# Kernel tuning notes

Measured on AMD Instinct MI355X. Metric: run time of the kernel, lower is better.

The kernel has to match this reference:

```python
import jax, jax.numpy as jnp
import numpy as np

N, E, D_IN, H, NSEG, SEG = 40000, 640000, 127, 128, 512, 64
D0 = D_IN + 1  # node features + batch-indicator column


def setup_inputs() -> dict:
    ks = jax.random.split(jax.random.key(0), 12)
    def w(k, i, o):
        return jax.random.normal(k, (i, o), jnp.float32) / np.float32(np.sqrt(i))
    return dict(
        x=jax.random.normal(ks[0], (N, D_IN), jnp.float32),
        ei=jax.random.randint(ks[1], (2, E), 0, N, jnp.int32),
        ew=jax.random.uniform(ks[2], (E,), jnp.float32),
        batches=jax.random.randint(ks[3], (NSEG * SEG,), 0, N, jnp.int32),
        lens=jnp.arange(NSEG + 1, dtype=jnp.int32) * SEG,  # CSR offsets, 512 segments of 64
        gin_w0=w(ks[4], D0, H), gin_b0=jnp.zeros((H,), jnp.float32),
        gin_w1=w(ks[5], H, H), gin_b1=jnp.zeros((H,), jnp.float32),
        gin_w2=w(ks[6], H, H), gin_b2=jnp.zeros((H,), jnp.float32),
        r_w1=w(ks[7], 3 * H, H), r_b1=jnp.zeros((H,), jnp.float32),
        ln1_g=jnp.ones((H,), jnp.float32), ln1_b=jnp.zeros((H,), jnp.float32),
        r_w2=w(ks[8], H, H), r_b2=jnp.zeros((H,), jnp.float32),
        ln2_g=jnp.ones((H,), jnp.float32), ln2_b=jnp.zeros((H,), jnp.float32),
        r_w3=w(ks[9], H, 1), r_b3=jnp.zeros((1,), jnp.float32),
    )


def _layernorm(v, g, b, eps=1e-5):
    m = jnp.mean(v, -1, keepdims=True)
    var = jnp.mean((v - m) ** 2, -1, keepdims=True)
    return (v - m) * jax.lax.rsqrt(var + eps) * g + b


def _gin_layer(h, src, dst, ew, w, b):
    # GINConv with eps=0: MLP((1+eps)*h + sum_{j->i} ew_ji * h_j), MLP = Linear+ReLU
    agg = jax.ops.segment_sum(ew[:, None] * h[src], dst, num_segments=N)
    return jax.nn.relu((h + agg) @ w + b)


def reference(x, ei, ew, batches, lens,
              gin_w0, gin_b0, gin_w1, gin_b1, gin_w2, gin_b2,
              r_w1, r_b1, ln1_g, ln1_b, r_w2, r_b2, ln2_g, ln2_b, r_w3, r_b3):
    src, dst = ei[0], ei[1]
    # batch indicator feature
    bf = jnp.zeros((N, 1), x.dtype).at[batches].set(1.0)
    h = jnp.concatenate([x, bf], axis=1)  # [N, D0]
    for w_, b_ in ((gin_w0, gin_b0), (gin_w1, gin_b1), (gin_w2, gin_b2)):
        h = _gin_layer(h, src, dst, ew, w_, b_)
    # MultiPool: gather per-subgraph nodes then mean/min/max segment reductions
    seg = jnp.searchsorted(lens, jnp.arange(NSEG * SEG, dtype=jnp.int32), side='right') - 1
    src_e = h[batches]  # [total, H]
    counts = (lens[1:] - lens[:-1]).astype(h.dtype)[:, None]
    mean_p = jax.ops.segment_sum(src_e, seg, num_segments=NSEG) / counts
    min_p = jax.ops.segment_min(src_e, seg, num_segments=NSEG)
    max_p = jax.ops.segment_max(src_e, seg, num_segments=NSEG)
    z = jnp.concatenate([mean_p, min_p, max_p], axis=1)  # [NSEG, 3H]
    # readout: Linear, ReLU, LN, Linear, LN, ReLU, Linear
    z = _layernorm(jax.nn.relu(z @ r_w1 + r_b1), ln1_g, ln1_b)
    z = jax.nn.relu(_layernorm(z @ r_w2 + r_b2, ln2_g, ln2_b))
    return z @ r_w3 + r_b3  # logits [NSEG, 1]
```

## Files before the change

kernel.cpp:

```cpp
#include <hip/hip_runtime.h>
#include <hip/hip_fp16.h>

#define NN   40000
#define EE   640000
#define DIN  127
#define HH   128
#define NSEGS 512
#define SEGSZ 64
#define CAP  64
#define NB_ELL 625
#define NB_H0  10000

typedef unsigned int uint;
typedef unsigned short ushort;
typedef _Float16 f16;
typedef __attribute__((ext_vector_type(8))) _Float16 f16x8;
typedef __attribute__((ext_vector_type(4))) float f32x4;

__device__ __forceinline__ float h2f_lo(uint v) {
    __half_raw r; r.x = (ushort)(v & 0xffff); return __half2float(__half(r));
}
__device__ __forceinline__ float h2f_hi(uint v) {
    __half_raw r; r.x = (ushort)(v >> 16); return __half2float(__half(r));
}
__device__ __forceinline__ ushort f2h(float f) {
    return __half_as_ushort(__float2half(f));
}

__global__ __launch_bounds__(256) void prep(int4* __restrict__ cnt4,
                                            const float* __restrict__ w0,
                                            const float* __restrict__ w1,
                                            const float* __restrict__ w2,
                                            ushort* __restrict__ wp) {
    int t = blockIdx.x * 256 + threadIdx.x;
    if (t < NN * 4) cnt4[t] = make_int4(0, 0, 0, 0);
    if (t < 3 * HH * HH) {
        int l = t / (HH * HH);
        int r = t - l * (HH * HH);
        int n = r >> 7, k = r & 127;
        const float* w = (l == 0) ? w0 : (l == 1) ? w1 : w2;
        wp[t] = f2h(w[k * HH + n]);
    }
}

__global__ __launch_bounds__(256) void ell_h0(const int* __restrict__ ei,
                                              const float* __restrict__ ew,
                                              int* __restrict__ cnt,
                                              uint* __restrict__ ell,
                                              const float* __restrict__ x,
                                              uint* __restrict__ h) {
    int b = blockIdx.x;
    if (b < NB_ELL) {
        int e = (b * 256 + threadIdx.x) * 4;
        int d0 = ei[EE + e + 0], d1 = ei[EE + e + 1];
        int d2 = ei[EE + e + 2], d3 = ei[EE + e + 3];
        int s0 = ei[e + 0], s1 = ei[e + 1], s2 = ei[e + 2], s3 = ei[e + 3];
        float w0 = ew[e + 0], w1 = ew[e + 1], w2 = ew[e + 2], w3 = ew[e + 3];
        int a0 = atomicAdd(&cnt[d0 << 4], 1);
        int a1 = atomicAdd(&cnt[d1 << 4], 1);
        int a2 = atomicAdd(&cnt[d2 << 4], 1);
        int a3 = atomicAdd(&cnt[d3 << 4], 1);
        if (a0 < CAP) ell[(size_t)d0 * CAP + a0] = (uint)s0 | ((uint)f2h(w0) << 16);
        if (a1 < CAP) ell[(size_t)d1 * CAP + a1] = (uint)s1 | ((uint)f2h(w1) << 16);
        if (a2 < CAP) ell[(size_t)d2 * CAP + a2] = (uint)s2 | ((uint)f2h(w2) << 16);
        if (a3 < CAP) ell[(size_t)d3 * CAP + a3] = (uint)s3 | ((uint)f2h(w3) << 16);
    } else {
        int t = (b - NB_ELL) * 256 + threadIdx.x;
        int i = t >> 6, q = t & 63;
        int d0 = q << 1;
        float a = x[i * DIN + d0];
        float bb = (d0 + 1 < DIN) ? x[i * DIN + d0 + 1] : 0.f;
        h[t] = (uint)f2h(a) | ((uint)f2h(bb) << 16);
    }
}

__global__ void set_bf(const int* __restrict__ batches, ushort* __restrict__ h) {
    int j = blockIdx.x * 256 + threadIdx.x;
    if (j < NSEGS * SEGSZ) h[(size_t)batches[j] * HH + DIN] = 0x3C00;
}

__global__ __launch_bounds__(256) void gin_agg(const uint* __restrict__ h,
                                               const int* __restrict__ cnt,
                                               const uint* __restrict__ ell,
                                               uint* __restrict__ tb) {
    int tid = threadIdx.x;
    int wid = tid >> 6;
    int lane = tid & 63;
    int half = lane >> 5;
    int l32 = lane & 31;
    int node = blockIdx.x * 8 + wid * 2 + half;
    int n = cnt[node << 4];
    if (n > CAP) n = CAP;
    const uint* row = ell + (size_t)node * CAP;
    uint2 self = *(const uint2*)(h + (size_t)node * 64 + l32 * 2);
    float ax = h2f_lo(self.x), ay = h2f_hi(self.x);
    float az = h2f_lo(self.y), aw = h2f_hi(self.y);
    float bx = 0.f, by = 0.f, bz = 0.f, bw = 0.f;
    int p = 0;
    for (; p + 4 <= n; p += 4) {
        uint4 ee = *(const uint4*)(row + p);
        uint2 v0 = *(const uint2*)(h + (size_t)(ee.x & 0xffff) * 64 + l32 * 2);
        uint2 v1 = *(const uint2*)(h + (size_t)(ee.y & 0xffff) * 64 + l32 * 2);
        uint2 v2 = *(const uint2*)(h + (size_t)(ee.z & 0xffff) * 64 + l32 * 2);
        uint2 v3 = *(const uint2*)(h + (size_t)(ee.w & 0xffff) * 64 + l32 * 2);
        float w0 = h2f_hi(ee.x), w1 = h2f_hi(ee.y);
        float w2 = h2f_hi(ee.z), w3 = h2f_hi(ee.w);
        ax += w0 * h2f_lo(v0.x); ay += w0 * h2f_hi(v0.x);
        az += w0 * h2f_lo(v0.y); aw += w0 * h2f_hi(v0.y);
        bx += w1 * h2f_lo(v1.x); by += w1 * h2f_hi(v1.x);
        bz += w1 * h2f_lo(v1.y); bw += w1 * h2f_hi(v1.y);
        ax += w2 * h2f_lo(v2.x); ay += w2 * h2f_hi(v2.x);
        az += w2 * h2f_lo(v2.y); aw += w2 * h2f_hi(v2.y);
        bx += w3 * h2f_lo(v3.x); by += w3 * h2f_hi(v3.x);
        bz += w3 * h2f_lo(v3.y); bw += w3 * h2f_hi(v3.y);
    }
    for (; p < n; ++p) {
        uint e = row[p];
        float w = h2f_hi(e);
        uint2 v = *(const uint2*)(h + (size_t)(e & 0xffff) * 64 + l32 * 2);
        ax += w * h2f_lo(v.x); ay += w * h2f_hi(v.x);
        az += w * h2f_lo(v.y); aw += w * h2f_hi(v.y);
    }
    ax += bx; ay += by; az += bz; aw += bw;
    uint2 o;
    o.x = (uint)f2h(ax) | ((uint)f2h(ay) << 16);
    o.y = (uint)f2h(az) | ((uint)f2h(aw) << 16);
    *(uint2*)(tb + (size_t)node * 64 + l32 * 2) = o;
}

__global__ __launch_bounds__(256) void gemm_mfma(const f16* __restrict__ tb,
                                                 const ushort* __restrict__ wp,
                                                 const float* __restrict__ bias,
                                                 ushort* __restrict__ hout) {
    int tid = threadIdx.x;
    int wave = tid >> 6, lane = tid & 63;
    int row0 = blockIdx.x * 64 + wave * 16;
    int n16 = lane & 15;
    int kg = lane >> 4;

    const f16* arow = tb + (size_t)(row0 + n16) * HH + kg * 8;
    f16x8 a0 = *(const f16x8*)(arow + 0);
    f16x8 a1 = *(const f16x8*)(arow + 32);
    f16x8 a2 = *(const f16x8*)(arow + 64);
    f16x8 a3 = *(const f16x8*)(arow + 96);

#pragma unroll
    for (int ct = 0; ct < 8; ct++) {
        const f16* brow = (const f16*)wp + (size_t)(ct * 16 + n16) * HH + kg * 8;
        f16x8 b0 = *(const f16x8*)(brow + 0);
        f16x8 b1 = *(const f16x8*)(brow + 32);
        f16x8 b2 = *(const f16x8*)(brow + 64);
        f16x8 b3 = *(const f16x8*)(brow + 96);
        f32x4 c = {0.f, 0.f, 0.f, 0.f};
        c = __builtin_amdgcn_mfma_f32_16x16x32_f16(a0, b0, c, 0, 0, 0);
        c = __builtin_amdgcn_mfma_f32_16x16x32_f16(a1, b1, c, 0, 0, 0);
        c = __builtin_amdgcn_mfma_f32_16x16x32_f16(a2, b2, c, 0, 0, 0);
        c = __builtin_amdgcn_mfma_f32_16x16x32_f16(a3, b3, c, 0, 0, 0);
        float bv = bias[ct * 16 + n16];
#pragma unroll
        for (int j = 0; j < 4; j++) {
            float o = fmaxf(c[j] + bv, 0.f);
            hout[(size_t)(row0 + kg * 4 + j) * HH + ct * 16 + n16] = f2h(o);
        }
    }
}

__device__ __forceinline__ float block_sum(float v, float* red, int c) {
    red[c] = v;
    __syncthreads();
#pragma unroll
    for (int off = 64; off > 0; off >>= 1) {
        if (c < off) red[c] += red[c + off];
        __syncthreads();
    }
    float r = red[0];
    __syncthreads();
    return r;
}

__global__ __launch_bounds__(128) void pool_readout(const ushort* __restrict__ h,
    const int* __restrict__ batches,
    const float* __restrict__ w1, const float* __restrict__ b1,
    const float* __restrict__ g1, const float* __restrict__ be1,
    const float* __restrict__ w2, const float* __restrict__ b2,
    const float* __restrict__ g2, const float* __restrict__ be2,
    const float* __restrict__ w3, const float* __restrict__ b3,
    float* __restrict__ out) {
    __shared__ float zr[384];
    __shared__ float red[128];
    __shared__ float v1[128];
    int s = blockIdx.x, c = threadIdx.x;

    float sum = 0.f, mn = INFINITY, mx = -INFINITY;
    for (int j = 0; j < SEGSZ; j++) {
        int idx = batches[s * SEGSZ + j];
        __half_raw r; r.x = h[(size_t)idx * HH + c];
        float v = __half2float(__half(r));
        sum += v;
        mn = fminf(mn, v);
        mx = fmaxf(mx, v);
    }
    zr[c] = sum * (1.f / SEGSZ);
    zr[128 + c] = mn;
    zr[256 + c] = mx;
    __syncthreads();

    float a = b1[c];
    for (int k = 0; k < 384; k++) a += zr[k] * w1[k * HH + c];
    a = fmaxf(a, 0.f);
    float m = block_sum(a, red, c) * (1.f / HH);
    float d = a - m;
    float var = block_sum(d * d, red, c) * (1.f / HH);
    float v = d * rsqrtf(var + 1e-5f) * g1[c] + be1[c];
    v1[c] = v;
    __syncthreads();

    float a2 = b2[c];
    for (int k = 0; k < HH; k++) a2 += v1[k] * w2[k * HH + c];
    float m2 = block_sum(a2, red, c) * (1.f / HH);
    float d2 = a2 - m2;
    float var2 = block_sum(d2 * d2, red, c) * (1.f / HH);
    float t2 = d2 * rsqrtf(var2 + 1e-5f) * g2[c] + be2[c];
    float z2 = fmaxf(t2, 0.f);

    float tot = block_sum(z2 * w3[c], red, c);
    if (c == 0) out[s] = tot + b3[0];
}

extern "C" void kernel_launch(void* const* d_in, const int* in_sizes, int n_in,
                              void* d_out, int out_size, void* d_ws, size_t ws_size,
                              hipStream_t stream) {
    const float* x        = (const float*)d_in[0];
    const int*   ei       = (const int*)d_in[1];
    const float* ew       = (const float*)d_in[2];
    const int*   batches  = (const int*)d_in[3];
    const float* gw[3]    = {(const float*)d_in[5], (const float*)d_in[7], (const float*)d_in[9]};
    const float* gb[3]    = {(const float*)d_in[6], (const float*)d_in[8], (const float*)d_in[10]};
    const float* r_w1 = (const float*)d_in[11]; const float* r_b1 = (const float*)d_in[12];
    const float* ln1g = (const float*)d_in[13]; const float* ln1b = (const float*)d_in[14];
    const float* r_w2 = (const float*)d_in[15]; const float* r_b2 = (const float*)d_in[16];
    const float* ln2g = (const float*)d_in[17]; const float* ln2b = (const float*)d_in[18];
    const float* r_w3 = (const float*)d_in[19]; const float* r_b3 = (const float*)d_in[20];
    float* out = (float*)d_out;

    uint*  h0   = (uint*)d_ws;
    uint*  h1   = h0 + (size_t)NN * 64;
    uint*  tb   = h1 + (size_t)NN * 64;
    uint*  wpk  = tb + (size_t)NN * 64;
    uint*  ell  = wpk + 3 * HH * HH / 2;
    int*   cnt  = (int*)(ell + (size_t)NN * CAP);

    prep<<<625, 256, 0, stream>>>((int4*)cnt, gw[0], gw[1], gw[2], (ushort*)wpk);
    ell_h0<<<NB_ELL + NB_H0, 256, 0, stream>>>(ei, ew, cnt, ell, x, h0);
    set_bf<<<(NSEGS * SEGSZ + 255) / 256, 256, 0, stream>>>(batches, (ushort*)h0);

    uint* hin = h0;
    uint* hout = h1;
    for (int l = 0; l < 3; l++) {
        gin_agg<<<NN / 8, 256, 0, stream>>>(hin, cnt, ell, tb);
        gemm_mfma<<<NN / 64, 256, 0, stream>>>((const f16*)tb,
                                               (const ushort*)wpk + (size_t)l * HH * HH,
                                               gb[l], (ushort*)hout);
        uint* tmp = hin; hin = hout; hout = tmp;
    }

    pool_readout<<<NSEGS, 128, 0, stream>>>((const ushort*)hin, batches,
                                            r_w1, r_b1, ln1g, ln1b,
                                            r_w2, r_b2, ln2g, ln2b, r_w3, r_b3, out);
}
```

Baseline: 188.8 us.

## Fuse GIN neighbor aggregation with MFMA linear layer via swizzled LDS tile

Merges the aggregation kernel and the GEMM kernel into one per-layer kernel. Each block aggregates 16 nodes into a swizzled shared-memory tile and then runs the 16x128 MFMA against the weights, with each wave handling two column tiles. This removes the global round-trip of the intermediate aggregated buffer and one launch per layer. In exchange, each block now reloads the full weight matrix for only 16 rows, and a block barrier separates the gather phase from the MFMA phase.

```diff
diff --git a/kernel.cpp b/kernel.cpp
--- a/kernel.cpp
+++ b/kernel.cpp
@@ -79,83 +79,83 @@
     if (j < NSEGS * SEGSZ) h[(size_t)batches[j] * HH + DIN] = 0x3C00;
 }
 
-__global__ __launch_bounds__(256) void gin_agg(const uint* __restrict__ h,
-                                               const int* __restrict__ cnt,
-                                               const uint* __restrict__ ell,
-                                               uint* __restrict__ tb) {
-    int tid = threadIdx.x;
-    int wid = tid >> 6;
-    int lane = tid & 63;
-    int half = lane >> 5;
-    int l32 = lane & 31;
-    int node = blockIdx.x * 8 + wid * 2 + half;
-    int n = cnt[node << 4];
-    if (n > CAP) n = CAP;
-    const uint* row = ell + (size_t)node * CAP;
-    uint2 self = *(const uint2*)(h + (size_t)node * 64 + l32 * 2);
-    float ax = h2f_lo(self.x), ay = h2f_hi(self.x);
-    float az = h2f_lo(self.y), aw = h2f_hi(self.y);
-    float bx = 0.f, by = 0.f, bz = 0.f, bw = 0.f;
-    int p = 0;
-    for (; p + 4 <= n; p += 4) {
-        uint4 ee = *(const uint4*)(row + p);
-        uint2 v0 = *(const uint2*)(h + (size_t)(ee.x & 0xffff) * 64 + l32 * 2);
-        uint2 v1 = *(const uint2*)(h + (size_t)(ee.y & 0xffff) * 64 + l32 * 2);
-        uint2 v2 = *(const uint2*)(h + (size_t)(ee.z & 0xffff) * 64 + l32 * 2);
-        uint2 v3 = *(const uint2*)(h + (size_t)(ee.w & 0xffff) * 64 + l32 * 2);
-        float w0 = h2f_hi(ee.x), w1 = h2f_hi(ee.y);
-        float w2 = h2f_hi(ee.z), w3 = h2f_hi(ee.w);
-        ax += w0 * h2f_lo(v0.x); ay += w0 * h2f_hi(v0.x);
-        az += w0 * h2f_lo(v0.y); aw += w0 * h2f_hi(v0.y);
-        bx += w1 * h2f_lo(v1.x); by += w1 * h2f_hi(v1.x);
-        bz += w1 * h2f_lo(v1.y); bw += w1 * h2f_hi(v1.y);
-        ax += w2 * h2f_lo(v2.x); ay += w2 * h2f_hi(v2.x);
-        az += w2 * h2f_lo(v2.y); aw += w2 * h2f_hi(v2.y);
-        bx += w3 * h2f_lo(v3.x); by += w3 * h2f_hi(v3.x);
-        bz += w3 * h2f_lo(v3.y); bw += w3 * h2f_hi(v3.y);
-    }
-    for (; p < n; ++p) {
-        uint e = row[p];
-        float w = h2f_hi(e);
-        uint2 v = *(const uint2*)(h + (size_t)(e & 0xffff) * 64 + l32 * 2);
-        ax += w * h2f_lo(v.x); ay += w * h2f_hi(v.x);
-        az += w * h2f_lo(v.y); aw += w * h2f_hi(v.y);
-    }
-    ax += bx; ay += by; az += bz; aw += bw;
-    uint2 o;
-    o.x = (uint)f2h(ax) | ((uint)f2h(ay) << 16);
-    o.y = (uint)f2h(az) | ((uint)f2h(aw) << 16);
-    *(uint2*)(tb + (size_t)node * 64 + l32 * 2) = o;
-}
-
-__global__ __launch_bounds__(256) void gemm_mfma(const f16* __restrict__ tb,
+__global__ __launch_bounds__(256) void gin_layer(const uint* __restrict__ h,
+                                                 const int* __restrict__ cnt,
+                                                 const uint* __restrict__ ell,
                                                  const ushort* __restrict__ wp,
                                                  const float* __restrict__ bias,
                                                  ushort* __restrict__ hout) {
+    __shared__ __align__(16) uint lds[16 * 64];
     int tid = threadIdx.x;
     int wave = tid >> 6, lane = tid & 63;
-    int row0 = blockIdx.x * 64 + wave * 16;
-    int n16 = lane & 15;
-    int kg = lane >> 4;
-
-    const f16* arow = tb + (size_t)(row0 + n16) * HH + kg * 8;
-    f16x8 a0 = *(const f16x8*)(arow + 0);
-    f16x8 a1 = *(const f16x8*)(arow + 32);
-    f16x8 a2 = *(const f16x8*)(arow + 64);
-    f16x8 a3 = *(const f16x8*)(arow + 96);
-
-#pragma unroll
-    for (int ct = 0; ct < 8; ct++) {
+    int half = lane >> 5, l32 = lane & 31;
+
+#pragma unroll
+    for (int it = 0; it < 2; ++it) {
+        int ni = it * 8 + wave * 2 + half;
+        int node = blockIdx.x * 16 + ni;
+        int n = cnt[node << 4];
+        if (n > CAP) n = CAP;
+        const uint* row = ell + (size_t)node * CAP;
+        uint2 self = *(const uint2*)(h + (size_t)node * 64 + l32 * 2);
+        float ax = h2f_lo(self.x), ay = h2f_hi(self.x);
+        float az = h2f_lo(self.y), aw = h2f_hi(self.y);
+        float bx = 0.f, by = 0.f, bz = 0.f, bw = 0.f;
+        int p = 0;
+        for (; p + 4 <= n; p += 4) {
+            uint4 ee = *(const uint4*)(row + p);
+            uint2 v0 = *(const uint2*)(h + (size_t)(ee.x & 0xffff) * 64 + l32 * 2);
+            uint2 v1 = *(const uint2*)(h + (size_t)(ee.y & 0xffff) * 64 + l32 * 2);
+            uint2 v2 = *(const uint2*)(h + (size_t)(ee.z & 0xffff) * 64 + l32 * 2);
+            uint2 v3 = *(const uint2*)(h + (size_t)(ee.w & 0xffff) * 64 + l32 * 2);
+            float w0 = h2f_hi(ee.x), w1 = h2f_hi(ee.y);
+            float w2 = h2f_hi(ee.z), w3 = h2f_hi(ee.w);
+            ax += w0 * h2f_lo(v0.x); ay += w0 * h2f_hi(v0.x);
+            az += w0 * h2f_lo(v0.y); aw += w0 * h2f_hi(v0.y);
+            bx += w1 * h2f_lo(v1.x); by += w1 * h2f_hi(v1.x);
+            bz += w1 * h2f_lo(v1.y); bw += w1 * h2f_hi(v1.y);
+            ax += w2 * h2f_lo(v2.x); ay += w2 * h2f_hi(v2.x);
+            az += w2 * h2f_lo(v2.y); aw += w2 * h2f_hi(v2.y);
+            bx += w3 * h2f_lo(v3.x); by += w3 * h2f_hi(v3.x);
+            bz += w3 * h2f_lo(v3.y); bw += w3 * h2f_hi(v3.y);
+        }
+        for (; p < n; ++p) {
+            uint e = row[p];
+            float w = h2f_hi(e);
+            uint2 v = *(const uint2*)(h + (size_t)(e & 0xffff) * 64 + l32 * 2);
+            ax += w * h2f_lo(v.x); ay += w * h2f_hi(v.x);
+            az += w * h2f_lo(v.y); aw += w * h2f_hi(v.y);
+        }
+        ax += bx; ay += by; az += bz; aw += bw;
+        uint2 o;
+        o.x = (uint)f2h(ax) | ((uint)f2h(ay) << 16);
+        o.y = (uint)f2h(az) | ((uint)f2h(aw) << 16);
+        int wsw = (l32 * 2) ^ ((ni & 7) << 2);
+        *(uint2*)(&lds[ni * 64 + wsw]) = o;
+    }
+    __syncthreads();
+
+    int n16 = lane & 15, kg = lane >> 4;
+    f16x8 a[4];
+#pragma unroll
+    for (int s = 0; s < 4; ++s) {
+        int w = (s * 16 + kg * 4) ^ ((n16 & 7) << 2);
+        a[s] = *(const f16x8*)(&lds[n16 * 64 + w]);
+    }
+    int row0 = blockIdx.x * 16;
+#pragma unroll
+    for (int t = 0; t < 2; ++t) {
+        int ct = wave * 2 + t;
         const f16* brow = (const f16*)wp + (size_t)(ct * 16 + n16) * HH + kg * 8;
         f16x8 b0 = *(const f16x8*)(brow + 0);
         f16x8 b1 = *(const f16x8*)(brow + 32);
         f16x8 b2 = *(const f16x8*)(brow + 64);
         f16x8 b3 = *(const f16x8*)(brow + 96);
         f32x4 c = {0.f, 0.f, 0.f, 0.f};
-        c = __builtin_amdgcn_mfma_f32_16x16x32_f16(a0, b0, c, 0, 0, 0);
-        c = __builtin_amdgcn_mfma_f32_16x16x32_f16(a1, b1, c, 0, 0, 0);
-        c = __builtin_amdgcn_mfma_f32_16x16x32_f16(a2, b2, c, 0, 0, 0);
-        c = __builtin_amdgcn_mfma_f32_16x16x32_f16(a3, b3, c, 0, 0, 0);
+        c = __builtin_amdgcn_mfma_f32_16x16x32_f16(a[0], b0, c, 0, 0, 0);
+        c = __builtin_amdgcn_mfma_f32_16x16x32_f16(a[1], b1, c, 0, 0, 0);
+        c = __builtin_amdgcn_mfma_f32_16x16x32_f16(a[2], b2, c, 0, 0, 0);
+        c = __builtin_amdgcn_mfma_f32_16x16x32_f16(a[3], b3, c, 0, 0, 0);
         float bv = bias[ct * 16 + n16];
 #pragma unroll
         for (int j = 0; j < 4; j++) {
@@ -245,8 +245,7 @@
 
     uint*  h0   = (uint*)d_ws;
     uint*  h1   = h0 + (size_t)NN * 64;
-    uint*  tb   = h1 + (size_t)NN * 64;
-    uint*  wpk  = tb + (size_t)NN * 64;
+    uint*  wpk  = h1 + (size_t)NN * 64;
     uint*  ell  = wpk + 3 * HH * HH / 2;
     int*   cnt  = (int*)(ell + (size_t)NN * CAP);
 
@@ -257,8 +256,7 @@
     uint* hin = h0;
     uint* hout = h1;
     for (int l = 0; l < 3; l++) {
-        gin_agg<<<NN / 8, 256, 0, stream>>>(hin, cnt, ell, tb);
-        gemm_mfma<<<NN / 64, 256, 0, stream>>>((const f16*)tb,
+        gin_layer<<<NN / 16, 256, 0, stream>>>(hin, cnt, ell,
                                                (const ushort*)wpk + (size_t)l * HH * HH,
                                                gb[l], (ushort*)hout);
         uint* tmp = hin; hin = hout; hout = tmp;
```

After: 185.3 us. No clear change (-1.8%).

## Partition gather columns across XCDs so each L2 caches a quarter of features

Applied to the files above, without the earlier changes.

Rewrites the GIN aggregation so each block handles 16 nodes and one quarter of the feature columns, with the quarter chosen from the block's XCD index. Each XCD's L2 then only holds a quarter of the node feature matrix, which fits in cache and reduces random-gather misses to HBM. In exchange, the edge lists and counts are read four times and each gathered segment shrinks to 64 bytes.

```diff
diff --git a/kernel.cpp b/kernel.cpp
--- a/kernel.cpp
+++ b/kernel.cpp
@@ -79,53 +79,48 @@
     if (j < NSEGS * SEGSZ) h[(size_t)batches[j] * HH + DIN] = 0x3C00;
 }
 
-__global__ __launch_bounds__(256) void gin_agg(const uint* __restrict__ h,
-                                               const int* __restrict__ cnt,
-                                               const uint* __restrict__ ell,
-                                               uint* __restrict__ tb) {
-    int tid = threadIdx.x;
-    int wid = tid >> 6;
-    int lane = tid & 63;
-    int half = lane >> 5;
-    int l32 = lane & 31;
-    int node = blockIdx.x * 8 + wid * 2 + half;
+__global__ __launch_bounds__(256) void gin_gather(const uint* __restrict__ h,
+                                                  const int* __restrict__ cnt,
+                                                  const uint* __restrict__ ell,
+                                                  uint* __restrict__ tb) {
+    int bid = blockIdx.x;
+    int xcd = bid & 7;
+    int q = xcd >> 1;
+    int chunk = (bid >> 3) * 2 + (xcd & 1);
+    int g = threadIdx.x >> 4;
+    int l16 = threadIdx.x & 15;
+    int node = chunk * 16 + g;
+    int colu = q * 16 + l16;
+
     int n = cnt[node << 4];
     if (n > CAP) n = CAP;
     const uint* row = ell + (size_t)node * CAP;
-    uint2 self = *(const uint2*)(h + (size_t)node * 64 + l32 * 2);
-    float ax = h2f_lo(self.x), ay = h2f_hi(self.x);
-    float az = h2f_lo(self.y), aw = h2f_hi(self.y);
-    float bx = 0.f, by = 0.f, bz = 0.f, bw = 0.f;
+    uint self = h[(size_t)node * 64 + colu];
+    float ax = h2f_lo(self), ay = h2f_hi(self);
+    float bx = 0.f, by = 0.f;
     int p = 0;
     for (; p + 4 <= n; p += 4) {
         uint4 ee = *(const uint4*)(row + p);
-        uint2 v0 = *(const uint2*)(h + (size_t)(ee.x & 0xffff) * 64 + l32 * 2);
-        uint2 v1 = *(const uint2*)(h + (size_t)(ee.y & 0xffff) * 64 + l32 * 2);
-        uint2 v2 = *(const uint2*)(h + (size_t)(ee.z & 0xffff) * 64 + l32 * 2);
-        uint2 v3 = *(const uint2*)(h + (size_t)(ee.w & 0xffff) * 64 + l32 * 2);
+        uint v0 = h[(size_t)(ee.x & 0xffff) * 64 + colu];
+        uint v1 = h[(size_t)(ee.y & 0xffff) * 64 + colu];
+        uint v2 = h[(size_t)(ee.z & 0xffff) * 64 + colu];
+        uint v3 = h[(size_t)(ee.w & 0xffff) * 64 + colu];
         float w0 = h2f_hi(ee.x), w1 = h2f_hi(ee.y);
         float w2 = h2f_hi(ee.z), w3 = h2f_hi(ee.w);
-        ax += w0 * h2f_lo(v0.x); ay += w0 * h2f_hi(v0.x);
-        az += w0 * h2f_lo(v0.y); aw += w0 * h2f_hi(v0.y);
-        bx += w1 * h2f_lo(v1.x); by += w1 * h2f_hi(v1.x);
-        bz += w1 * h2f_lo(v1.y); bw += w1 * h2f_hi(v1.y);
-        ax += w2 * h2f_lo(v2.x); ay += w2 * h2f_hi(v2.x);
-        az += w2 * h2f_lo(v2.y); aw += w2 * h2f_hi(v2.y);
-        bx += w3 * h2f_lo(v3.x); by += w3 * h2f_hi(v3.x);
-        bz += w3 * h2f_lo(v3.y); bw += w3 * h2f_hi(v3.y);
+        ax += w0 * h2f_lo(v0); ay += w0 * h2f_hi(v0);
+        bx += w1 * h2f_lo(v1); by += w1 * h2f_hi(v1);
+        ax += w2 * h2f_lo(v2); ay += w2 * h2f_hi(v2);
+        bx += w3 * h2f_lo(v3); by += w3 * h2f_hi(v3);
     }
     for (; p < n; ++p) {
         uint e = row[p];
         float w = h2f_hi(e);
-        uint2 v = *(const uint2*)(h + (size_t)(e & 0xffff) * 64 + l32 * 2);
-        ax += w * h2f_lo(v.x); ay += w * h2f_hi(v.x);
-        az += w * h2f_lo(v.y); aw += w * h2f_hi(v.y);
-    }
-    ax += bx; ay += by; az += bz; aw += bw;
-    uint2 o;
-    o.x = (uint)f2h(ax) | ((uint)f2h(ay) << 16);
-    o.y = (uint)f2h(az) | ((uint)f2h(aw) << 16);
-    *(uint2*)(tb + (size_t)node * 64 + l32 * 2) = o;
+        uint v = h[(size_t)(e & 0xffff) * 64 + colu];
+        ax += w * h2f_lo(v);
+        ay += w * h2f_hi(v);
+    }
+    ax += bx; ay += by;
+    tb[(size_t)node * 64 + colu] = (uint)f2h(ax) | ((uint)f2h(ay) << 16);
 }
 
 __global__ __launch_bounds__(256) void gemm_mfma(const f16* __restrict__ tb,
@@ -257,7 +252,7 @@
     uint* hin = h0;
     uint* hout = h1;
     for (int l = 0; l < 3; l++) {
-        gin_agg<<<NN / 8, 256, 0, stream>>>(hin, cnt, ell, tb);
+        gin_gather<<<NN / 16 * 4, 256, 0, stream>>>(hin, cnt, ell, tb);
         gemm_mfma<<<NN / 64, 256, 0, stream>>>((const f16*)tb,
                                                (const ushort*)wpk + (size_t)l * HH * HH,
                                                gb[l], (ushort*)hout);
```

Result: slower. 230.6 us (+22.2%).
